# Performance work log

Hardware: AMD Instinct MI355X
Metric: run time of the kernel (lower is better)

The kernel has to match this reference:

```python
import jax, jax.numpy as jnp
import numpy as np

WS = (3, 8, 8)          # (t, h, w) window
SHIFT = (0, 4, 4)
HEADS = 6
DIM = 120
HD = DIM // HEADS
SCALE = HD ** -0.5
N = WS[0] * WS[1] * WS[2]   # 192 tokens per window
NQ = N // 3                 # 64 query tokens (last frame)


def _rel_pos_index():
    cd, ch, cw = np.arange(WS[0]), np.arange(WS[1]), np.arange(WS[2])
    c2 = np.stack(np.meshgrid(cd, ch, cw, indexing='ij')).reshape(3, -1)      # (3, N)
    c1 = np.stack(np.meshgrid(np.arange(1), ch, cw, indexing='ij')).reshape(3, -1)  # (3, NQ)
    rel = (c1[:, :, None] - c2[:, None, :]).transpose(1, 2, 0)                # (NQ, N, 3)
    rel = rel + np.array([WS[0] - 1, WS[1] - 1, WS[2] - 1])
    idx = rel[..., 0] * (2 * WS[1] - 1) * (2 * WS[2] - 1) + rel[..., 1] * (2 * WS[2] - 1) + rel[..., 2]
    return idx.astype(np.int32)  # values in [0, 3*15*15)


def _shift_attn_mask(h, w):
    # standard Swin shifted-window mask, tiled over the 3 frames
    img = np.zeros((h, w), np.int32)
    cnt = 0
    for hs in (slice(0, -WS[1]), slice(-WS[1], -SHIFT[1]), slice(-SHIFT[1], None)):
        for ws_ in (slice(0, -WS[2]), slice(-WS[2], -SHIFT[2]), slice(-SHIFT[2], None)):
            img[hs, ws_] = cnt
            cnt += 1
    win = img.reshape(h // WS[1], WS[1], w // WS[2], WS[2]).transpose(0, 2, 1, 3).reshape(-1, WS[1] * WS[2])
    m2 = win[:, None, :] - win[:, :, None]
    m2 = np.where(m2 != 0, -100.0, 0.0).astype(np.float32)  # (nW, 64, 64)
    return np.tile(m2, (1, 3, 3))                            # (nW, 192, 192)


def setup_inputs() -> dict:
    key = jax.random.key(0)
    ks = jax.random.split(key, 10)
    b, t, h, w, c = 1, 3, 256, 256, DIM
    nW = (h // WS[1]) * (w // WS[2])
    B_ = b * nW
    return {
        'x': jax.random.normal(ks[0], (b, t, h, w, c), jnp.float32),
        'quary0': jax.random.normal(ks[1], (B_, NQ, c), jnp.float32),
        'quary1': jax.random.normal(ks[2], (B_, NQ, c), jnp.float32),
        'qkv_w': jax.random.normal(ks[3], (3 * c, c), jnp.float32) * 0.02,
        'qkv_b': jnp.zeros((3 * c,), jnp.float32),
        'proj_w': jax.random.normal(ks[4], (c, c), jnp.float32) * 0.02,
        'proj_b': jnp.zeros((c,), jnp.float32),
        'rpb_table': jax.random.normal(ks[5], (WS[0] * (2 * WS[1] - 1) * (2 * WS[2] - 1), HEADS), jnp.float32) * 0.02,
        'pm_w': jax.random.normal(ks[6], (1, c), jnp.float32) * 0.02,
        'pm_b': jnp.zeros((1,), jnp.float32),
        'attn_mask': jnp.asarray(_shift_attn_mask(h, w)),
        'rel_idx': jnp.asarray(_rel_pos_index()),
    }


def reference(x, quary0, quary1, qkv_w, qkv_b, proj_w, proj_b, rpb_table, pm_w, pm_b, attn_mask, rel_idx):
    b, t, h, w, c = x.shape
    # cyclic shift
    x = jnp.roll(x, (-SHIFT[0], -SHIFT[1], -SHIFT[2]), axis=(1, 2, 3))
    # window partition -> (B_, N, c)
    xw = x.reshape(b, t // WS[0], WS[0], h // WS[1], WS[1], w // WS[2], WS[2], c)
    xw = xw.transpose(0, 1, 3, 5, 2, 4, 6, 7).reshape(-1, N, c)
    B_ = xw.shape[0]
    # adaptive mask prediction (eval path: hard threshold; sigmoid(s/T)>=0.5 <=> s>=0)
    pred_q = jax.lax.stop_gradient(xw[:, 2 * NQ:, :])
    soft = jnp.abs(pred_q - quary0) @ pm_w.T + pm_b          # (B_, NQ, 1)
    pred = (soft >= 0).astype(x.dtype)
    # qkv
    qkv = (xw @ qkv_w.T + qkv_b).reshape(B_, N, 3, HEADS, HD).transpose(2, 0, 3, 1, 4)
    q = qkv[0][:, :, 2 * NQ:, :] * SCALE                      # (B_, H, NQ, hd)
    k, v = qkv[1], qkv[2]                                     # (B_, H, N, hd)
    attn = jnp.einsum('bhqd,bhkd->bhqk', q, k)                # (B_, H, NQ, N)
    # gathered relative position bias
    rpb = rpb_table[rel_idx.reshape(-1)].reshape(NQ, N, HEADS).transpose(2, 0, 1)
    attn = attn + rpb[None]
    # shift mask
    nW = attn_mask.shape[0]
    attn = attn.reshape(b, nW, HEADS, NQ, N) + attn_mask[None, :, None, 2 * NQ:, :]
    attn = jax.nn.softmax(attn.reshape(B_, HEADS, NQ, N), axis=-1)
    out = jnp.einsum('bhqk,bhkd->bqhd', attn, v).reshape(B_, NQ, c)
    # output projection + token-pruning blend (math-equivalent to gather/fill eval path)
    x1 = out @ proj_w.T + proj_b
    x_pred = x1 * pred + quary1 * (1.0 - pred)
    xo = jnp.concatenate([x_pred, pred], axis=-1)             # (B_, NQ, c+1)
    # single-frame window reverse
    xo = xo.reshape(b, h // WS[1], w // WS[2], WS[1], WS[2], c + 1)
    xo = xo.transpose(0, 1, 3, 2, 4, 5).reshape(b, h, w, c + 1)
    xo = jnp.roll(xo, (SHIFT[1], SHIFT[2]), axis=(1, 2))
    return xo
```

## Files before the change

kernel.cpp:

```cpp
#include <hip/hip_runtime.h>
#include <math.h>

#define NT 256

typedef __attribute__((ext_vector_type(8))) short s16x8;
typedef __attribute__((ext_vector_type(4))) float f32x4;

#define KVF_OFF 0
#define QF_OFF  73728
#define PJF_OFF 122880
#define RPB_OFF 172032

__device__ __forceinline__ unsigned short f2bf(float f) {
    union { float f; unsigned int i; } v; v.f = f;
    unsigned int x = v.i;
    x += 0x7fffu + ((x >> 16) & 1u);
    return (unsigned short)(x >> 16);
}
__device__ __forceinline__ unsigned int pk2(float a, float b) {
    return (unsigned int)f2bf(a) | ((unsigned int)f2bf(b) << 16);
}

#define MFMA(a, b, c) __builtin_amdgcn_mfma_f32_16x16x32_bf16(a, b, c, 0, 0, 0)

__global__ void prep(const float* __restrict__ qkv_w,
                     const float* __restrict__ proj_w,
                     const float* __restrict__ rpb_table,
                     const int*   __restrict__ rel_idx,
                     unsigned char* __restrict__ wsb)
{
    int gid = blockIdx.x * blockDim.x + threadIdx.x;
    int nthr = gridDim.x * blockDim.x;
    unsigned short* KVF = (unsigned short*)(wsb + KVF_OFF);
    unsigned short* QF  = (unsigned short*)(wsb + QF_OFF);
    unsigned short* PJF = (unsigned short*)(wsb + PJF_OFF);
    float*          RPB = (float*)(wsb + RPB_OFF);

    for (int f = gid; f < 6 * 3 * 4 * 512; f += nthr) {
        int q = f & 511, rest = f >> 9;
        int kk = rest & 3, rest2 = rest >> 2;
        int nt = rest2 % 3, h = rest2 / 3;
        int ln = q >> 3, j = q & 7;
        int l15 = ln & 15, qd = ln >> 4;
        int nglob = nt * 16 + l15, k = kk * 32 + qd * 8 + j;
        float v = 0.f;
        if (k < 120 && nglob < 40) {
            int row = (nglob < 20) ? (120 + h * 20 + nglob) : (240 + h * 20 + nglob - 20);
            v = qkv_w[row * 120 + k];
        }
        KVF[f] = f2bf(v);
    }
    for (int f = gid; f < 6 * 2 * 4 * 512; f += nthr) {
        int q = f & 511, rest = f >> 9;
        int kk = rest & 3, rest2 = rest >> 2;
        int nt = rest2 & 1, h = rest2 >> 1;
        int ln = q >> 3, j = q & 7;
        int l15 = ln & 15, qd = ln >> 4;
        int nn = nt * 16 + l15, k = kk * 32 + qd * 8 + j;
        int row = h * 20 + nn;
        float v = (k < 120) ? qkv_w[row * 120 + k] : 0.f;
        QF[f] = f2bf(v);
    }
    for (int f = gid; f < 6 * 8 * 512; f += nthr) {
        int q = f & 511, rest = f >> 9;
        int ct = rest & 7, h = rest >> 3;
        int ln = q >> 3, j = q & 7;
        int l15 = ln & 15, qd = ln >> 4;
        int c = ct * 16 + l15, k = qd * 8 + j;
        float v = (k < 20 && c < 120) ? proj_w[c * 120 + h * 20 + k] : 0.f;
        PJF[f] = f2bf(v);
    }
    for (int i = gid; i < 6 * 192 * 64; i += nthr) {
        int r = i & 63, n = (i >> 6) % 192, h = i / (192 * 64);
        RPB[i] = rpb_table[rel_idx[r * 192 + n] * 6 + h];
    }
}

__global__ __launch_bounds__(NT, 2)
void swin_mfma(const float* __restrict__ x,
               const float* __restrict__ quary0,
               const float* __restrict__ quary1,
               const float* __restrict__ qkv_b,
               const float* __restrict__ proj_b,
               const float* __restrict__ pm_w,
               const float* __restrict__ pm_b,
               const unsigned char* __restrict__ wsb,
               float* __restrict__ out)
{
    __shared__ alignas(16) unsigned char smem[79888];
    unsigned short* xw = (unsigned short*)smem;
    unsigned short* ks = (unsigned short*)(smem + 46096);
    unsigned short* vt = (unsigned short*)(smem + 61456);
    unsigned short* qs = (unsigned short*)(smem + 74256);
    float* pred_s = (float*)(smem + 79376);
    int*   grp_s  = (int*)(smem + 79632);

    const int tid = threadIdx.x;
    const int wv = tid >> 6, ln = tid & 63;
    const int l15 = ln & 15, qd = ln >> 4;
    const int widx = blockIdx.x;
    const int wh = widx >> 5, ww = widx & 31;
    const float SCALE = 0.22360679774997896f;

    const unsigned short* KVF = (const unsigned short*)(wsb + KVF_OFF);
    const unsigned short* QF  = (const unsigned short*)(wsb + QF_OFF);
    const unsigned short* PJF = (const unsigned short*)(wsb + PJF_OFF);
    const float*          RPB = (const float*)(wsb + RPB_OFF);

    for (int e = tid; e < 192 * 30; e += NT) {
        int n = e / 30, c4 = e % 30;
        int f = n >> 6, ii = (n >> 3) & 7, jj = n & 7;
        int y0 = (wh * 8 + ii + 4) & 255;
        int x0 = (ww * 8 + jj + 4) & 255;
        float4 val = *(const float4*)(x + (((size_t)(f * 256 + y0)) * 256 + x0) * 120 + c4 * 4);
        unsigned int lo = (unsigned)f2bf(val.x) | ((unsigned)f2bf(val.y) << 16);
        unsigned int hi = (unsigned)f2bf(val.z) | ((unsigned)f2bf(val.w) << 16);
        unsigned int off = (unsigned)(n * 120 + c4 * 4);
        *(unsigned int*)(xw + off)     = lo;
        *(unsigned int*)(xw + off + 2) = hi;
    }
    if (tid < 8) xw[192 * 120 + tid] = 0;
    for (int e = tid; e < 192 * 12; e += NT) ks[(e / 12) * 40 + 20 + (e % 12)] = 0;
    for (int e = tid; e < 64 * 12;  e += NT) qs[(e / 12) * 40 + 20 + (e % 12)] = 0;
    for (int e = tid; e < 12 * 200; e += NT) vt[(20 + e / 200) * 200 + (e % 200)] = 0;
    if (tid < 64) {
        int ii = tid >> 3, jj = tid & 7;
        int y0 = (wh * 8 + ii + 4) & 255;
        int x0 = (ww * 8 + jj + 4) & 255;
        int hg = (y0 >= 248) + (y0 >= 252);
        int wg = (x0 >= 248) + (x0 >= 252);
        grp_s[tid] = hg * 3 + wg;
    }
    {
        int r = tid >> 2, j = tid & 3;
        int ii = r >> 3, jj = r & 7;
        int y0 = (wh * 8 + ii + 4) & 255;
        int x0 = (ww * 8 + jj + 4) & 255;
        const float* xr  = x + (((size_t)(2 * 256 + y0)) * 256 + x0) * 120;
        const float* q0r = quary0 + ((size_t)widx * 64 + r) * 120;
        float acc = 0.f;
        for (int ch = j * 30; ch < j * 30 + 30; ++ch)
            acc += fabsf(xr[ch] - q0r[ch]) * pm_w[ch];
        acc += __shfl_xor(acc, 1);
        acc += __shfl_xor(acc, 2);
        if (j == 0) pred_s[r] = (acc + pm_b[0] >= 0.f) ? 1.f : 0.f;
    }
    __syncthreads();

    const int q_l = wv * 16 + l15;
    const int gq = grp_s[q_l];
    unsigned long long mbits = 0ull;
    #pragma unroll
    for (int t = 0; t < 12; ++t)
        #pragma unroll
        for (int r = 0; r < 4; ++r) {
            int tok = t * 16 + qd * 4 + r;
            if (gq != grp_s[tok & 63]) mbits |= (1ull << (t * 4 + r));
        }
    const int srcA = (((qd * 2) & 3) << 4) | l15;
    const int srcB = (((qd * 2 + 1) & 3) << 4) | l15;
    const int msel = qd >> 1;

    f32x4 pacc[8];
    #pragma unroll
    for (int i = 0; i < 8; ++i) { f32x4 z = {0.f,0.f,0.f,0.f}; pacc[i] = z; }

    for (int h = 0; h < 6; ++h) {
        for (int e = wv; e < 44; e += 4) {
            if (e < 36) {
                int mt = e % 12, nt = e / 12;
                const unsigned short* arow  = xw + (mt * 16 + l15) * 120;
                const unsigned short* bbase = KVF + ((h * 3 + nt) * 4) * 512 + ln * 8;
                f32x4 acc = {0.f, 0.f, 0.f, 0.f};
                #pragma unroll
                for (int kk = 0; kk < 4; ++kk) {
                    s16x8 aF = *(const s16x8*)(arow + kk * 32 + qd * 8);
                    s16x8 bF = *(const s16x8*)(bbase + kk * 512);
                    acc = MFMA(aF, bF, acc);
                }
                int nglob = nt * 16 + l15;
                if (nglob < 40) {
                    float bias = qkv_b[nglob < 20 ? (120 + h * 20 + nglob)
                                                  : (240 + h * 20 + nglob - 20)];
                    #pragma unroll
                    for (int reg = 0; reg < 4; ++reg) {
                        int tok = mt * 16 + qd * 4 + reg;
                        unsigned short vb = f2bf(acc[reg] + bias);
                        if (nglob < 20) ks[tok * 40 + nglob] = vb;
                        else            vt[(nglob - 20) * 200 + tok] = vb;
                    }
                }
            } else {
                int t = e - 36, mt = t & 3, nt = t >> 2;
                const unsigned short* arow  = xw + (128 + mt * 16 + l15) * 120;
                const unsigned short* bbase = QF + ((h * 2 + nt) * 4) * 512 + ln * 8;
                f32x4 acc = {0.f, 0.f, 0.f, 0.f};
                #pragma unroll
                for (int kk = 0; kk < 4; ++kk) {
                    s16x8 aF = *(const s16x8*)(arow + kk * 32 + qd * 8);
                    s16x8 bF = *(const s16x8*)(bbase + kk * 512);
                    acc = MFMA(aF, bF, acc);
                }
                int nn = nt * 16 + l15;
                if (nn < 20) {
                    float bias = qkv_b[h * 20 + nn];
                    #pragma unroll
                    for (int reg = 0; reg < 4; ++reg)
                        qs[(mt * 16 + qd * 4 + reg) * 40 + nn] = f2bf((acc[reg] + bias) * SCALE);
                }
            }
        }
        __syncthreads();

        const float* rbase = RPB + ((size_t)(h * 192 + qd * 4)) * 64 + q_l;
        float vals[48];
        #pragma unroll
        for (int t = 0; t < 12; ++t)
            #pragma unroll
            for (int r = 0; r < 4; ++r)
                vals[t * 4 + r] = rbase[(t * 16 + r) * 64]
                                + (((mbits >> (t * 4 + r)) & 1ull) ? -100.f : 0.f);

        const s16x8 bQ = *(const s16x8*)(qs + q_l * 40 + qd * 8);
        f32x4 sc[12];
        #pragma unroll
        for (int t = 0; t < 12; ++t) {
            s16x8 aK = *(const s16x8*)(ks + (t * 16 + l15) * 40 + qd * 8);
            f32x4 z = {0.f, 0.f, 0.f, 0.f};
            sc[t] = MFMA(aK, bQ, z);
        }

        float m = -1e30f;
        #pragma unroll
        for (int t = 0; t < 12; ++t)
            #pragma unroll
            for (int r = 0; r < 4; ++r) {
                float v = vals[t * 4 + r] + sc[t][r];
                vals[t * 4 + r] = v; m = fmaxf(m, v);
            }
        m = fmaxf(m, __shfl_xor(m, 16));
        m = fmaxf(m, __shfl_xor(m, 32));
        float s = 0.f;
        #pragma unroll
        for (int i = 0; i < 48; ++i) { float ev = __expf(vals[i] - m); vals[i] = ev; s += ev; }
        s += __shfl_xor(s, 16);
        s += __shfl_xor(s, 32);
        float inv = 1.0f / s;

        unsigned int plo[12], phi[12];
        #pragma unroll
        for (int t = 0; t < 12; ++t) {
            plo[t] = pk2(vals[t * 4 + 0] * inv, vals[t * 4 + 1] * inv);
            phi[t] = pk2(vals[t * 4 + 2] * inv, vals[t * 4 + 3] * inv);
        }

        f32x4 o0 = {0.f,0.f,0.f,0.f}, o1 = {0.f,0.f,0.f,0.f};
        #pragma unroll
        for (int kk = 0; kk < 6; ++kk) {
            unsigned int a0 = __shfl(plo[2 * kk],     srcA);
            unsigned int a1 = __shfl(plo[2 * kk + 1], srcA);
            unsigned int b0 = __shfl(phi[2 * kk],     srcA);
            unsigned int b1 = __shfl(phi[2 * kk + 1], srcA);
            unsigned int c0 = __shfl(plo[2 * kk],     srcB);
            unsigned int c1 = __shfl(plo[2 * kk + 1], srcB);
            unsigned int d0 = __shfl(phi[2 * kk],     srcB);
            unsigned int d1 = __shfl(phi[2 * kk + 1], srcB);
            union { s16x8 v; unsigned int u[4]; } bf;
            bf.u[0] = msel ? a1 : a0;
            bf.u[1] = msel ? b1 : b0;
            bf.u[2] = msel ? c1 : c0;
            bf.u[3] = msel ? d1 : d0;
            s16x8 aV0 = *(const s16x8*)(vt + l15 * 200 + kk * 32 + qd * 8);
            s16x8 aV1 = *(const s16x8*)(vt + (16 + l15) * 200 + kk * 32 + qd * 8);
            o0 = MFMA(aV0, bf.v, o0);
            o1 = MFMA(aV1, bf.v, o1);
        }

        {
            unsigned int ol0 = pk2(o0[0], o0[1]), oh0 = pk2(o0[2], o0[3]);
            unsigned int ol1 = pk2(o1[0], o1[1]), oh1 = pk2(o1[2], o1[3]);
            unsigned int w0a = __shfl(ol0, srcA), w0b = __shfl(ol1, srcA);
            unsigned int w1a = __shfl(oh0, srcA), w1b = __shfl(oh1, srcA);
            unsigned int w2a = __shfl(ol0, srcB), w2b = __shfl(ol1, srcB);
            unsigned int w3a = __shfl(oh0, srcB), w3b = __shfl(oh1, srcB);
            union { s16x8 v; unsigned int u[4]; } bo;
            bo.u[0] = msel ? w0b : w0a;
            bo.u[1] = msel ? w1b : w1a;
            bo.u[2] = msel ? w2b : w2a;
            bo.u[3] = msel ? w3b : w3a;
            #pragma unroll
            for (int ct = 0; ct < 8; ++ct) {
                s16x8 aP = *(const s16x8*)(PJF + (h * 8 + ct) * 512 + ln * 8);
                pacc[ct] = MFMA(aP, bo.v, pacc[ct]);
            }
        }
        __syncthreads();
    }

    float* xo = (float*)smem;
    #pragma unroll
    for (int ct = 0; ct < 8; ++ct)
        #pragma unroll
        for (int r = 0; r < 4; ++r) {
            int c = ct * 16 + qd * 4 + r;
            if (c < 120) xo[q_l * 129 + c] = pacc[ct][r];
        }
    __syncthreads();

    for (int e = tid; e < 64 * 121; e += NT) {
        int r = e / 121, c = e - r * 121;
        int ii = r >> 3, jj = r & 7;
        int y0 = (wh * 8 + ii + 4) & 255;
        int x0 = (ww * 8 + jj + 4) & 255;
        float p = pred_s[r];
        float val;
        if (c < 120)
            val = (p != 0.f) ? (xo[r * 129 + c] + proj_b[c])
                             : quary1[(size_t)widx * 7680 + (size_t)r * 120 + c];
        else
            val = p;
        out[((size_t)(y0 * 256 + x0)) * 121 + c] = val;
    }
}

extern "C" void kernel_launch(void* const* d_in, const int* in_sizes, int n_in,
                              void* d_out, int out_size, void* d_ws, size_t ws_size,
                              hipStream_t stream) {
    const float* x        = (const float*)d_in[0];
    const float* quary0   = (const float*)d_in[1];
    const float* quary1   = (const float*)d_in[2];
    const float* qkv_w    = (const float*)d_in[3];
    const float* qkv_b    = (const float*)d_in[4];
    const float* proj_w   = (const float*)d_in[5];
    const float* proj_b   = (const float*)d_in[6];
    const float* rpb      = (const float*)d_in[7];
    const float* pm_w     = (const float*)d_in[8];
    const float* pm_b     = (const float*)d_in[9];
    const int*   rel_idx  = (const int*)d_in[11];
    float* out = (float*)d_out;
    unsigned char* wsb = (unsigned char*)d_ws;

    prep<<<128, 512, 0, stream>>>(qkv_w, proj_w, rpb, rel_idx, wsb);
    swin_mfma<<<1024, NT, 0, stream>>>(x, quary0, quary1, qkv_b, proj_b,
                                       pm_w, pm_b, wsb, out);
}
```

Measured before the change: 457.8 us.

## Hoist QKV projection for all heads before attention and split heads across waves

Q, K and V are now projected for all six heads in one upfront MFMA pass into large LDS buffers, replacing the per-head projection loop that needed two block syncs per head. The softmax scale is folded into the Q weights and bias. The block doubles to 512 threads, with two wave groups each taking three heads. Their projection partial sums are written to two LDS tiles and added in the epilogue. LDS grows to about 159KB, and launch_bounds(512,2) may squeeze registers, so there is a risk of spills or lost occupancy.

```diff
diff --git a/kernel.cpp b/kernel.cpp
--- a/kernel.cpp
+++ b/kernel.cpp
@@ -1,15 +1,17 @@
 #include <hip/hip_runtime.h>
 #include <math.h>
 
-#define NT 256
+#define NT 512
 
 typedef __attribute__((ext_vector_type(8))) short s16x8;
+typedef __attribute__((ext_vector_type(4))) short s16x4;
 typedef __attribute__((ext_vector_type(4))) float f32x4;
 
-#define KVF_OFF 0
-#define QF_OFF  73728
-#define PJF_OFF 122880
-#define RPB_OFF 172032
+#define WKT_OFF 0
+#define WVT_OFF 32768
+#define WQT_OFF 65536
+#define PJF_OFF 102400
+#define RPB_OFF 151552
 
 __device__ __forceinline__ unsigned short f2bf(float f) {
     union { float f; unsigned int i; } v; v.f = f;
@@ -31,41 +33,42 @@
 {
     int gid = blockIdx.x * blockDim.x + threadIdx.x;
     int nthr = gridDim.x * blockDim.x;
-    unsigned short* KVF = (unsigned short*)(wsb + KVF_OFF);
-    unsigned short* QF  = (unsigned short*)(wsb + QF_OFF);
+    unsigned short* WKT = (unsigned short*)(wsb + WKT_OFF);
+    unsigned short* WVT = (unsigned short*)(wsb + WVT_OFF);
+    unsigned short* WQT = (unsigned short*)(wsb + WQT_OFF);
     unsigned short* PJF = (unsigned short*)(wsb + PJF_OFF);
     float*          RPB = (float*)(wsb + RPB_OFF);
 
-    for (int f = gid; f < 6 * 3 * 4 * 512; f += nthr) {
+    for (int f = gid; f < 8 * 4 * 512; f += nthr) {
         int q = f & 511, rest = f >> 9;
-        int kk = rest & 3, rest2 = rest >> 2;
-        int nt = rest2 % 3, h = rest2 / 3;
-        int ln = q >> 3, j = q & 7;
-        int l15 = ln & 15, qd = ln >> 4;
-        int nglob = nt * 16 + l15, k = kk * 32 + qd * 8 + j;
-        float v = 0.f;
-        if (k < 120 && nglob < 40) {
-            int row = (nglob < 20) ? (120 + h * 20 + nglob) : (240 + h * 20 + nglob - 20);
-            v = qkv_w[row * 120 + k];
-        }
-        KVF[f] = f2bf(v);
-    }
-    for (int f = gid; f < 6 * 2 * 4 * 512; f += nthr) {
+        int kk = rest & 3, nt = rest >> 2;
+        int ln = q >> 3, j = q & 7, l15 = ln & 15, qd = ln >> 4;
+        int c = nt * 16 + l15, ch = kk * 32 + qd * 8 + j;
+        float v = (c < 120 && ch < 120) ? qkv_w[(120 + c) * 120 + ch] : 0.f;
+        WKT[f] = f2bf(v);
+    }
+    for (int f = gid; f < 8 * 4 * 512; f += nthr) {
         int q = f & 511, rest = f >> 9;
-        int kk = rest & 3, rest2 = rest >> 2;
-        int nt = rest2 & 1, h = rest2 >> 1;
-        int ln = q >> 3, j = q & 7;
-        int l15 = ln & 15, qd = ln >> 4;
-        int nn = nt * 16 + l15, k = kk * 32 + qd * 8 + j;
-        int row = h * 20 + nn;
-        float v = (k < 120) ? qkv_w[row * 120 + k] : 0.f;
-        QF[f] = f2bf(v);
+        int kk = rest & 3, mt = rest >> 2;
+        int ln = q >> 3, j = q & 7, l15 = ln & 15, qd = ln >> 4;
+        int d = mt * 16 + l15, ch = kk * 32 + qd * 8 + j;
+        float v = (d < 120 && ch < 120) ? qkv_w[(240 + d) * 120 + ch] : 0.f;
+        WVT[f] = f2bf(v);
+    }
+    for (int f = gid; f < 9 * 4 * 512; f += nthr) {
+        int q = f & 511, rest = f >> 9;
+        int kk = rest & 3, nt = rest >> 2;
+        int ln = q >> 3, j = q & 7, l15 = ln & 15, qd = ln >> 4;
+        int c = nt * 16 + l15, ch = kk * 32 + qd * 8 + j;
+        int hh = (c * 171) >> 12, rel = c - hh * 24;
+        float v = (rel < 20 && ch < 120)
+                    ? qkv_w[(hh * 20 + rel) * 120 + ch] * 0.22360679774997896f : 0.f;
+        WQT[f] = f2bf(v);
     }
     for (int f = gid; f < 6 * 8 * 512; f += nthr) {
         int q = f & 511, rest = f >> 9;
         int ct = rest & 7, h = rest >> 3;
-        int ln = q >> 3, j = q & 7;
-        int l15 = ln & 15, qd = ln >> 4;
+        int ln = q >> 3, j = q & 7, l15 = ln & 15, qd = ln >> 4;
         int c = ct * 16 + l15, k = qd * 8 + j;
         float v = (k < 20 && c < 120) ? proj_w[c * 120 + h * 20 + k] : 0.f;
         PJF[f] = f2bf(v);
@@ -87,23 +90,23 @@
                const unsigned char* __restrict__ wsb,
                float* __restrict__ out)
 {
-    __shared__ alignas(16) unsigned char smem[79888];
+    __shared__ alignas(16) unsigned char smem[159152];
     unsigned short* xw = (unsigned short*)smem;
-    unsigned short* ks = (unsigned short*)(smem + 46096);
-    unsigned short* vt = (unsigned short*)(smem + 61456);
-    unsigned short* qs = (unsigned short*)(smem + 74256);
-    float* pred_s = (float*)(smem + 79376);
-    int*   grp_s  = (int*)(smem + 79632);
+    unsigned short* kd = (unsigned short*)(smem + 46096);
+    unsigned short* vt = (unsigned short*)(smem + 92208);
+    unsigned short* qp = (unsigned short*)(smem + 140208);
+    float* pred_s = (float*)(smem + 158640);
+    int*   grp_s  = (int*)(smem + 158896);
 
     const int tid = threadIdx.x;
     const int wv = tid >> 6, ln = tid & 63;
     const int l15 = ln & 15, qd = ln >> 4;
     const int widx = blockIdx.x;
     const int wh = widx >> 5, ww = widx & 31;
-    const float SCALE = 0.22360679774997896f;
-
-    const unsigned short* KVF = (const unsigned short*)(wsb + KVF_OFF);
-    const unsigned short* QF  = (const unsigned short*)(wsb + QF_OFF);
+
+    const unsigned short* WKT = (const unsigned short*)(wsb + WKT_OFF);
+    const unsigned short* WVT = (const unsigned short*)(wsb + WVT_OFF);
+    const unsigned short* WQT = (const unsigned short*)(wsb + WQT_OFF);
     const unsigned short* PJF = (const unsigned short*)(wsb + PJF_OFF);
     const float*          RPB = (const float*)(wsb + RPB_OFF);
 
@@ -119,10 +122,8 @@
         *(unsigned int*)(xw + off)     = lo;
         *(unsigned int*)(xw + off + 2) = hi;
     }
-    if (tid < 8) xw[192 * 120 + tid] = 0;
-    for (int e = tid; e < 192 * 12; e += NT) ks[(e / 12) * 40 + 20 + (e % 12)] = 0;
-    for (int e = tid; e < 64 * 12;  e += NT) qs[(e / 12) * 40 + 20 + (e % 12)] = 0;
-    for (int e = tid; e < 12 * 200; e += NT) vt[(20 + e / 200) * 200 + (e % 200)] = 0;
+    if (tid < 8)  xw[192 * 120 + tid] = 0;
+    if (tid < 16) kd[192 * 120 + tid] = 0;
     if (tid < 64) {
         int ii = tid >> 3, jj = tid & 7;
         int y0 = (wh * 8 + ii + 4) & 255;
@@ -131,7 +132,7 @@
         int wg = (x0 >= 248) + (x0 >= 252);
         grp_s[tid] = hg * 3 + wg;
     }
-    {
+    if (tid < 256) {
         int r = tid >> 2, j = tid & 3;
         int ii = r >> 3, jj = r & 7;
         int y0 = (wh * 8 + ii + 4) & 255;
@@ -147,7 +148,71 @@
     }
     __syncthreads();
 
-    const int q_l = wv * 16 + l15;
+    for (int e = wv; e < 48; e += 8) {
+        int mt = e >> 2, ntp = e & 3;
+        const unsigned short* arow = xw + (mt * 16 + l15) * 120;
+        const unsigned short* b0 = WKT + (2 * ntp) * 4 * 512 + ln * 8;
+        f32x4 a0 = {0.f,0.f,0.f,0.f}, a1 = {0.f,0.f,0.f,0.f};
+        #pragma unroll
+        for (int kk = 0; kk < 4; ++kk) {
+            s16x8 aF = *(const s16x8*)(arow + kk * 32 + qd * 8);
+            a0 = MFMA(aF, *(const s16x8*)(b0 + kk * 512), a0);
+            a1 = MFMA(aF, *(const s16x8*)(b0 + 2048 + kk * 512), a1);
+        }
+        #pragma unroll
+        for (int half = 0; half < 2; ++half) {
+            int c = (2 * ntp + half) * 16 + l15;
+            f32x4 acc = half ? a1 : a0;
+            if (c < 120) {
+                float bias = qkv_b[120 + c];
+                #pragma unroll
+                for (int reg = 0; reg < 4; ++reg)
+                    kd[(mt * 16 + qd * 4 + reg) * 120 + c] = f2bf(acc[reg] + bias);
+            }
+        }
+    }
+    for (int e = wv; e < 48; e += 8) {
+        int nt = e >> 2, mtp = e & 3;
+        const unsigned short* brow = xw + (nt * 16 + l15) * 120;
+        const unsigned short* a0 = WVT + (2 * mtp) * 4 * 512 + ln * 8;
+        f32x4 c0 = {0.f,0.f,0.f,0.f}, c1 = {0.f,0.f,0.f,0.f};
+        #pragma unroll
+        for (int kk = 0; kk < 4; ++kk) {
+            s16x8 bF = *(const s16x8*)(brow + kk * 32 + qd * 8);
+            c0 = MFMA(*(const s16x8*)(a0 + kk * 512), bF, c0);
+            c1 = MFMA(*(const s16x8*)(a0 + 2048 + kk * 512), bF, c1);
+        }
+        #pragma unroll
+        for (int half = 0; half < 2; ++half) {
+            f32x4 acc = half ? c1 : c0;
+            #pragma unroll
+            for (int reg = 0; reg < 4; ++reg) {
+                int d = (2 * mtp + half) * 16 + qd * 4 + reg;
+                if (d < 120)
+                    vt[d * 200 + nt * 16 + l15] = f2bf(acc[reg] + qkv_b[240 + d]);
+            }
+        }
+    }
+    for (int e = wv; e < 36; e += 8) {
+        int mt = e / 9, nt = e - mt * 9;
+        const unsigned short* arow = xw + (128 + mt * 16 + l15) * 120;
+        const unsigned short* b0 = WQT + nt * 4 * 512 + ln * 8;
+        f32x4 acc = {0.f,0.f,0.f,0.f};
+        #pragma unroll
+        for (int kk = 0; kk < 4; ++kk)
+            acc = MFMA(*(const s16x8*)(arow + kk * 32 + qd * 8),
+                       *(const s16x8*)(b0 + kk * 512), acc);
+        int c = nt * 16 + l15;
+        int hh = (c * 171) >> 12, rel = c - hh * 24;
+        float bias = (rel < 20) ? qkv_b[hh * 20 + rel] * 0.22360679774997896f : 0.f;
+        #pragma unroll
+        for (int reg = 0; reg < 4; ++reg)
+            qp[(mt * 16 + qd * 4 + reg) * 144 + c] = f2bf(acc[reg] + bias);
+    }
+    __syncthreads();
+
+    const int qt = wv & 3, hp = wv >> 2;
+    const int q_l = qt * 16 + l15;
     const int gq = grp_s[q_l];
     unsigned long long mbits = 0ull;
     #pragma unroll
@@ -165,52 +230,8 @@
     #pragma unroll
     for (int i = 0; i < 8; ++i) { f32x4 z = {0.f,0.f,0.f,0.f}; pacc[i] = z; }
 
-    for (int h = 0; h < 6; ++h) {
-        for (int e = wv; e < 44; e += 4) {
-            if (e < 36) {
-                int mt = e % 12, nt = e / 12;
-                const unsigned short* arow  = xw + (mt * 16 + l15) * 120;
-                const unsigned short* bbase = KVF + ((h * 3 + nt) * 4) * 512 + ln * 8;
-                f32x4 acc = {0.f, 0.f, 0.f, 0.f};
-                #pragma unroll
-                for (int kk = 0; kk < 4; ++kk) {
-                    s16x8 aF = *(const s16x8*)(arow + kk * 32 + qd * 8);
-                    s16x8 bF = *(const s16x8*)(bbase + kk * 512);
-                    acc = MFMA(aF, bF, acc);
-                }
-                int nglob = nt * 16 + l15;
-                if (nglob < 40) {
-                    float bias = qkv_b[nglob < 20 ? (120 + h * 20 + nglob)
-                                                  : (240 + h * 20 + nglob - 20)];
-                    #pragma unroll
-                    for (int reg = 0; reg < 4; ++reg) {
-                        int tok = mt * 16 + qd * 4 + reg;
-                        unsigned short vb = f2bf(acc[reg] + bias);
-                        if (nglob < 20) ks[tok * 40 + nglob] = vb;
-                        else            vt[(nglob - 20) * 200 + tok] = vb;
-                    }
-                }
-            } else {
-                int t = e - 36, mt = t & 3, nt = t >> 2;
-                const unsigned short* arow  = xw + (128 + mt * 16 + l15) * 120;
-                const unsigned short* bbase = QF + ((h * 2 + nt) * 4) * 512 + ln * 8;
-                f32x4 acc = {0.f, 0.f, 0.f, 0.f};
-                #pragma unroll
-                for (int kk = 0; kk < 4; ++kk) {
-                    s16x8 aF = *(const s16x8*)(arow + kk * 32 + qd * 8);
-                    s16x8 bF = *(const s16x8*)(bbase + kk * 512);
-                    acc = MFMA(aF, bF, acc);
-                }
-                int nn = nt * 16 + l15;
-                if (nn < 20) {
-                    float bias = qkv_b[h * 20 + nn];
-                    #pragma unroll
-                    for (int reg = 0; reg < 4; ++reg)
-                        qs[(mt * 16 + qd * 4 + reg) * 40 + nn] = f2bf((acc[reg] + bias) * SCALE);
-                }
-            }
-        }
-        __syncthreads();
+    for (int jj = 0; jj < 3; ++jj) {
+        const int h = hp + 2 * jj;
 
         const float* rbase = RPB + ((size_t)(h * 192 + qd * 4)) * 64 + q_l;
         float vals[48];
@@ -221,13 +242,20 @@
                 vals[t * 4 + r] = rbase[(t * 16 + r) * 64]
                                 + (((mbits >> (t * 4 + r)) & 1ull) ? -100.f : 0.f);
 
-        const s16x8 bQ = *(const s16x8*)(qs + q_l * 40 + qd * 8);
+        s16x8 zf = {0,0,0,0,0,0,0,0};
+        int koff = (qd == 3) ? 0 : qd * 8;
+        s16x8 bQl = *(const s16x8*)(qp + q_l * 144 + h * 24 + koff);
+        s16x8 bQ = (qd == 3) ? zf : bQl;
+
         f32x4 sc[12];
         #pragma unroll
         for (int t = 0; t < 12; ++t) {
-            s16x8 aK = *(const s16x8*)(ks + (t * 16 + l15) * 40 + qd * 8);
-            f32x4 z = {0.f, 0.f, 0.f, 0.f};
-            sc[t] = MFMA(aK, bQ, z);
+            const unsigned short* kp = kd + (t * 16 + l15) * 120 + h * 20 + qd * 8;
+            union { s16x8 v8; s16x4 v4[2]; } ak;
+            ak.v4[0] = *(const s16x4*)(kp);
+            ak.v4[1] = *(const s16x4*)(kp + 4);
+            f32x4 z = {0.f,0.f,0.f,0.f};
+            sc[t] = MFMA(ak.v8, bQ, z);
         }
 
         float m = -1e30f;
@@ -270,8 +298,8 @@
             bf.u[1] = msel ? b1 : b0;
             bf.u[2] = msel ? c1 : c0;
             bf.u[3] = msel ? d1 : d0;
-            s16x8 aV0 = *(const s16x8*)(vt + l15 * 200 + kk * 32 + qd * 8);
-            s16x8 aV1 = *(const s16x8*)(vt + (16 + l15) * 200 + kk * 32 + qd * 8);
+            s16x8 aV0 = *(const s16x8*)(vt + (h * 20 + l15) * 200 + kk * 32 + qd * 8);
+            s16x8 aV1 = *(const s16x8*)(vt + (h * 20 + 16 + l15) * 200 + kk * 32 + qd * 8);
             o0 = MFMA(aV0, bf.v, o0);
             o1 = MFMA(aV1, bf.v, o1);
         }
@@ -294,19 +322,23 @@
                 pacc[ct] = MFMA(aP, bo.v, pacc[ct]);
             }
         }
-        __syncthreads();
-    }
-
-    float* xo = (float*)smem;
-    #pragma unroll
-    for (int ct = 0; ct < 8; ++ct)
-        #pragma unroll
-        for (int r = 0; r < 4; ++r) {
-            int c = ct * 16 + qd * 4 + r;
-            if (c < 120) xo[q_l * 129 + c] = pacc[ct][r];
-        }
+    }
     __syncthreads();
 
+    {
+        float* xo = (float*)(smem + ((wv < 4) ? 0u : 46096u));
+        #pragma unroll
+        for (int ct = 0; ct < 8; ++ct)
+            #pragma unroll
+            for (int reg = 0; reg < 4; ++reg) {
+                int c = ct * 16 + qd * 4 + reg;
+                if (c < 120) xo[q_l * 129 + c] = pacc[ct][reg];
+            }
+    }
+    __syncthreads();
+
+    const float* x1p = (const float*)smem;
+    const float* x2p = (const float*)(smem + 46096);
     for (int e = tid; e < 64 * 121; e += NT) {
         int r = e / 121, c = e - r * 121;
         int ii = r >> 3, jj = r & 7;
@@ -315,7 +347,7 @@
         float p = pred_s[r];
         float val;
         if (c < 120)
-            val = (p != 0.f) ? (xo[r * 129 + c] + proj_b[c])
+            val = (p != 0.f) ? (x1p[r * 129 + c] + x2p[r * 129 + c] + proj_b[c])
                              : quary1[(size_t)widx * 7680 + (size_t)r * 120 + c];
         else
             val = p;
@@ -331,8 +363,8 @@
     const float* quary1   = (const float*)d_in[2];
     const float* qkv_w    = (const float*)d_in[3];
     const float* qkv_b    = (const float*)d_in[4];
+    const float* proj_b   = (const float*)d_in[6];
     const float* proj_w   = (const float*)d_in[5];
-    const float* proj_b   = (const float*)d_in[6];
     const float* rpb      = (const float*)d_in[7];
     const float* pm_w     = (const float*)d_in[8];
     const float* pm_b     = (const float*)d_in[9];
```

Measured after the change: 561.6 us. 1.23x slower.

## Drop shared-memory x staging and read x from global inside QKV MFMA loop

Applied to the files above, without the earlier changes.

Removes the bf16 copy of the window's x tile from LDS and instead loads fp32 x directly from global memory inside the QKV projection, converting to bf16 per MFMA operand. This shrinks LDS from about 78KB to 33KB and raises launch bounds to four blocks per SM for higher occupancy. The trade-off is that x is reloaded and reconverted from global for every head and every N-tile (6 heads × 3 tiles for K/V, 6 heads × 2 tiles for Q), so global/L2 traffic and conversion ALU work rise substantially.

```diff
diff --git a/kernel.cpp b/kernel.cpp
--- a/kernel.cpp
+++ b/kernel.cpp
@@ -19,6 +19,14 @@
 }
 __device__ __forceinline__ unsigned int pk2(float a, float b) {
     return (unsigned int)f2bf(a) | ((unsigned int)f2bf(b) << 16);
+}
+__device__ __forceinline__ s16x8 cvt8(float4 a, float4 b) {
+    union { unsigned int u[4]; s16x8 v; } r;
+    r.u[0] = pk2(a.x, a.y);
+    r.u[1] = pk2(a.z, a.w);
+    r.u[2] = pk2(b.x, b.y);
+    r.u[3] = pk2(b.z, b.w);
+    return r.v;
 }
 
 #define MFMA(a, b, c) __builtin_amdgcn_mfma_f32_16x16x32_bf16(a, b, c, 0, 0, 0)
@@ -76,7 +84,7 @@
     }
 }
 
-__global__ __launch_bounds__(NT, 2)
+__global__ __launch_bounds__(NT, 4)
 void swin_mfma(const float* __restrict__ x,
                const float* __restrict__ quary0,
                const float* __restrict__ quary1,
@@ -87,13 +95,12 @@
                const unsigned char* __restrict__ wsb,
                float* __restrict__ out)
 {
-    __shared__ alignas(16) unsigned char smem[79888];
-    unsigned short* xw = (unsigned short*)smem;
-    unsigned short* ks = (unsigned short*)(smem + 46096);
-    unsigned short* vt = (unsigned short*)(smem + 61456);
-    unsigned short* qs = (unsigned short*)(smem + 74256);
-    float* pred_s = (float*)(smem + 79376);
-    int*   grp_s  = (int*)(smem + 79632);
+    __shared__ alignas(16) unsigned char smem[33792];
+    unsigned short* ks = (unsigned short*)smem;
+    unsigned short* vt = (unsigned short*)(smem + 15360);
+    unsigned short* qs = (unsigned short*)(smem + 28160);
+    float* pred_s = (float*)(smem + 33280);
+    int*   grp_s  = (int*)(smem + 33536);
 
     const int tid = threadIdx.x;
     const int wv = tid >> 6, ln = tid & 63;
@@ -107,19 +114,6 @@
     const unsigned short* PJF = (const unsigned short*)(wsb + PJF_OFF);
     const float*          RPB = (const float*)(wsb + RPB_OFF);
 
-    for (int e = tid; e < 192 * 30; e += NT) {
-        int n = e / 30, c4 = e % 30;
-        int f = n >> 6, ii = (n >> 3) & 7, jj = n & 7;
-        int y0 = (wh * 8 + ii + 4) & 255;
-        int x0 = (ww * 8 + jj + 4) & 255;
-        float4 val = *(const float4*)(x + (((size_t)(f * 256 + y0)) * 256 + x0) * 120 + c4 * 4);
-        unsigned int lo = (unsigned)f2bf(val.x) | ((unsigned)f2bf(val.y) << 16);
-        unsigned int hi = (unsigned)f2bf(val.z) | ((unsigned)f2bf(val.w) << 16);
-        unsigned int off = (unsigned)(n * 120 + c4 * 4);
-        *(unsigned int*)(xw + off)     = lo;
-        *(unsigned int*)(xw + off + 2) = hi;
-    }
-    if (tid < 8) xw[192 * 120 + tid] = 0;
     for (int e = tid; e < 192 * 12; e += NT) ks[(e / 12) * 40 + 20 + (e % 12)] = 0;
     for (int e = tid; e < 64 * 12;  e += NT) qs[(e / 12) * 40 + 20 + (e % 12)] = 0;
     for (int e = tid; e < 12 * 200; e += NT) vt[(20 + e / 200) * 200 + (e % 200)] = 0;
@@ -169,14 +163,21 @@
         for (int e = wv; e < 44; e += 4) {
             if (e < 36) {
                 int mt = e % 12, nt = e / 12;
-                const unsigned short* arow  = xw + (mt * 16 + l15) * 120;
+                int n = mt * 16 + l15;
+                int f = n >> 6, ii = (n >> 3) & 7, jj = n & 7;
+                int y0 = (wh * 8 + ii + 4) & 255;
+                int x0 = (ww * 8 + jj + 4) & 255;
+                const float* xr = x + (((size_t)(f * 256 + y0)) * 256 + x0) * 120;
                 const unsigned short* bbase = KVF + ((h * 3 + nt) * 4) * 512 + ln * 8;
                 f32x4 acc = {0.f, 0.f, 0.f, 0.f};
                 #pragma unroll
                 for (int kk = 0; kk < 4; ++kk) {
-                    s16x8 aF = *(const s16x8*)(arow + kk * 32 + qd * 8);
-                    s16x8 bF = *(const s16x8*)(bbase + kk * 512);
-                    acc = MFMA(aF, bF, acc);
+                    float4 va = {0.f,0.f,0.f,0.f}, vb = {0.f,0.f,0.f,0.f};
+                    if (!(kk == 3 && qd == 3)) {
+                        va = *(const float4*)(xr + kk * 32 + qd * 8);
+                        vb = *(const float4*)(xr + kk * 32 + qd * 8 + 4);
+                    }
+                    acc = MFMA(cvt8(va, vb), *(const s16x8*)(bbase + kk * 512), acc);
                 }
                 int nglob = nt * 16 + l15;
                 if (nglob < 40) {
@@ -185,21 +186,28 @@
                     #pragma unroll
                     for (int reg = 0; reg < 4; ++reg) {
                         int tok = mt * 16 + qd * 4 + reg;
-                        unsigned short vb = f2bf(acc[reg] + bias);
-                        if (nglob < 20) ks[tok * 40 + nglob] = vb;
-                        else            vt[(nglob - 20) * 200 + tok] = vb;
+                        unsigned short vbf = f2bf(acc[reg] + bias);
+                        if (nglob < 20) ks[tok * 40 + nglob] = vbf;
+                        else            vt[(nglob - 20) * 200 + tok] = vbf;
                     }
                 }
             } else {
                 int t = e - 36, mt = t & 3, nt = t >> 2;
-                const unsigned short* arow  = xw + (128 + mt * 16 + l15) * 120;
+                int n = 128 + mt * 16 + l15;
+                int f = n >> 6, ii = (n >> 3) & 7, jj = n & 7;
+                int y0 = (wh * 8 + ii + 4) & 255;
+                int x0 = (ww * 8 + jj + 4) & 255;
+                const float* xr = x + (((size_t)(f * 256 + y0)) * 256 + x0) * 120;
                 const unsigned short* bbase = QF + ((h * 2 + nt) * 4) * 512 + ln * 8;
                 f32x4 acc = {0.f, 0.f, 0.f, 0.f};
                 #pragma unroll
                 for (int kk = 0; kk < 4; ++kk) {
-                    s16x8 aF = *(const s16x8*)(arow + kk * 32 + qd * 8);
-                    s16x8 bF = *(const s16x8*)(bbase + kk * 512);
-                    acc = MFMA(aF, bF, acc);
+                    float4 va = {0.f,0.f,0.f,0.f}, vb = {0.f,0.f,0.f,0.f};
+                    if (!(kk == 3 && qd == 3)) {
+                        va = *(const float4*)(xr + kk * 32 + qd * 8);
+                        vb = *(const float4*)(xr + kk * 32 + qd * 8 + 4);
+                    }
+                    acc = MFMA(cvt8(va, vb), *(const s16x8*)(bbase + kk * 512), acc);
                 }
                 int nn = nt * 16 + l15;
                 if (nn < 20) {
```

Result: slower. 673.0 us (+47.0%).

## Software-pipeline per-head QKV projection with double-buffered V/Q in LDS

Applied to the files above, without the earlier changes.

Moves the QKV projection for head h+1 into the attention loop of head h. Q and V get double buffers, and the K tile is overwritten only after a barrier that follows the score MFMAs. This removes one barrier per head and overlaps the projection MFMAs with softmax and PV work. K and Q row strides shrink from 40 to 24 and the zero-padding is trimmed, which lowers LDS use. The risk is heavier register pressure and subtle ordering hazards on the shared K buffer.

```diff
diff --git a/kernel.cpp b/kernel.cpp
--- a/kernel.cpp
+++ b/kernel.cpp
@@ -87,13 +87,13 @@
                const unsigned char* __restrict__ wsb,
                float* __restrict__ out)
 {
-    __shared__ alignas(16) unsigned char smem[79888];
+    __shared__ alignas(16) unsigned char smem[77968];
     unsigned short* xw = (unsigned short*)smem;
     unsigned short* ks = (unsigned short*)(smem + 46096);
+    unsigned short* qs = (unsigned short*)(smem + 55312);
     unsigned short* vt = (unsigned short*)(smem + 61456);
-    unsigned short* qs = (unsigned short*)(smem + 74256);
-    float* pred_s = (float*)(smem + 79376);
-    int*   grp_s  = (int*)(smem + 79632);
+    float* pred_s = (float*)(smem + 77456);
+    int*   grp_s  = (int*)(smem + 77712);
 
     const int tid = threadIdx.x;
     const int wv = tid >> 6, ln = tid & 63;
@@ -113,16 +113,16 @@
         int y0 = (wh * 8 + ii + 4) & 255;
         int x0 = (ww * 8 + jj + 4) & 255;
         float4 val = *(const float4*)(x + (((size_t)(f * 256 + y0)) * 256 + x0) * 120 + c4 * 4);
-        unsigned int lo = (unsigned)f2bf(val.x) | ((unsigned)f2bf(val.y) << 16);
-        unsigned int hi = (unsigned)f2bf(val.z) | ((unsigned)f2bf(val.w) << 16);
+        unsigned int lo = pk2(val.x, val.y);
+        unsigned int hi = pk2(val.z, val.w);
         unsigned int off = (unsigned)(n * 120 + c4 * 4);
         *(unsigned int*)(xw + off)     = lo;
         *(unsigned int*)(xw + off + 2) = hi;
     }
     if (tid < 8) xw[192 * 120 + tid] = 0;
-    for (int e = tid; e < 192 * 12; e += NT) ks[(e / 12) * 40 + 20 + (e % 12)] = 0;
-    for (int e = tid; e < 64 * 12;  e += NT) qs[(e / 12) * 40 + 20 + (e % 12)] = 0;
-    for (int e = tid; e < 12 * 200; e += NT) vt[(20 + e / 200) * 200 + (e % 200)] = 0;
+    for (int e = tid; e < 192 * 4; e += NT) ks[(e >> 2) * 24 + 20 + (e & 3)] = 0;
+    for (int e = tid; e < 2 * 64 * 4; e += NT)
+        qs[(e >> 8) * 1536 + ((e >> 2) & 63) * 24 + 20 + (e & 3)] = 0;
     if (tid < 64) {
         int ii = tid >> 3, jj = tid & 7;
         int y0 = (wh * 8 + ii + 4) & 255;
@@ -147,6 +147,51 @@
     }
     __syncthreads();
 
+    auto kvjob = [&](int mt, int nt, int hh, int pty) {
+        const unsigned short* arow  = xw + (mt * 16 + l15) * 120;
+        const unsigned short* bbase = KVF + ((hh * 3 + nt) * 4) * 512 + ln * 8;
+        f32x4 acc = {0.f, 0.f, 0.f, 0.f};
+        #pragma unroll
+        for (int kk = 0; kk < 4; ++kk)
+            acc = MFMA(*(const s16x8*)(arow + kk * 32 + qd * 8),
+                       *(const s16x8*)(bbase + kk * 512), acc);
+        int nglob = nt * 16 + l15;
+        if (nglob < 40) {
+            float bias = qkv_b[nglob < 20 ? (120 + hh * 20 + nglob)
+                                          : (240 + hh * 20 + nglob - 20)];
+            #pragma unroll
+            for (int reg = 0; reg < 4; ++reg) {
+                int tok = mt * 16 + qd * 4 + reg;
+                unsigned short vb = f2bf(acc[reg] + bias);
+                if (nglob < 20) ks[tok * 24 + nglob] = vb;
+                else            vt[pty * 4000 + (nglob - 20) * 200 + tok] = vb;
+            }
+        }
+    };
+    auto qjob = [&](int mt, int nt, int hh, int pty) {
+        const unsigned short* arow  = xw + (128 + mt * 16 + l15) * 120;
+        const unsigned short* bbase = QF + ((hh * 2 + nt) * 4) * 512 + ln * 8;
+        f32x4 acc = {0.f, 0.f, 0.f, 0.f};
+        #pragma unroll
+        for (int kk = 0; kk < 4; ++kk)
+            acc = MFMA(*(const s16x8*)(arow + kk * 32 + qd * 8),
+                       *(const s16x8*)(bbase + kk * 512), acc);
+        int nn = nt * 16 + l15;
+        if (nn < 20) {
+            float bias = qkv_b[hh * 20 + nn];
+            #pragma unroll
+            for (int reg = 0; reg < 4; ++reg)
+                qs[pty * 1536 + (mt * 16 + qd * 4 + reg) * 24 + nn] =
+                    f2bf((acc[reg] + bias) * SCALE);
+        }
+    };
+
+    for (int e = wv; e < 44; e += 4) {
+        if (e < 36) kvjob(e % 12, e / 12, 0, 0);
+        else        { int t = e - 36; qjob(t & 3, t >> 2, 0, 0); }
+    }
+    __syncthreads();
+
     const int q_l = wv * 16 + l15;
     const int gq = grp_s[q_l];
     unsigned long long mbits = 0ull;
@@ -160,57 +205,14 @@
     const int srcA = (((qd * 2) & 3) << 4) | l15;
     const int srcB = (((qd * 2 + 1) & 3) << 4) | l15;
     const int msel = qd >> 1;
+    const s16x8 zf = {0, 0, 0, 0, 0, 0, 0, 0};
 
     f32x4 pacc[8];
     #pragma unroll
     for (int i = 0; i < 8; ++i) { f32x4 z = {0.f,0.f,0.f,0.f}; pacc[i] = z; }
 
     for (int h = 0; h < 6; ++h) {
-        for (int e = wv; e < 44; e += 4) {
-            if (e < 36) {
-                int mt = e % 12, nt = e / 12;
-                const unsigned short* arow  = xw + (mt * 16 + l15) * 120;
-                const unsigned short* bbase = KVF + ((h * 3 + nt) * 4) * 512 + ln * 8;
-                f32x4 acc = {0.f, 0.f, 0.f, 0.f};
-                #pragma unroll
-                for (int kk = 0; kk < 4; ++kk) {
-                    s16x8 aF = *(const s16x8*)(arow + kk * 32 + qd * 8);
-                    s16x8 bF = *(const s16x8*)(bbase + kk * 512);
-                    acc = MFMA(aF, bF, acc);
-                }
-                int nglob = nt * 16 + l15;
-                if (nglob < 40) {
-                    float bias = qkv_b[nglob < 20 ? (120 + h * 20 + nglob)
-                                                  : (240 + h * 20 + nglob - 20)];
-                    #pragma unroll
-                    for (int reg = 0; reg < 4; ++reg) {
-                        int tok = mt * 16 + qd * 4 + reg;
-                        unsigned short vb = f2bf(acc[reg] + bias);
-                        if (nglob < 20) ks[tok * 40 + nglob] = vb;
-                        else            vt[(nglob - 20) * 200 + tok] = vb;
-                    }
-                }
-            } else {
-                int t = e - 36, mt = t & 3, nt = t >> 2;
-                const unsigned short* arow  = xw + (128 + mt * 16 + l15) * 120;
-                const unsigned short* bbase = QF + ((h * 2 + nt) * 4) * 512 + ln * 8;
-                f32x4 acc = {0.f, 0.f, 0.f, 0.f};
-                #pragma unroll
-                for (int kk = 0; kk < 4; ++kk) {
-                    s16x8 aF = *(const s16x8*)(arow + kk * 32 + qd * 8);
-                    s16x8 bF = *(const s16x8*)(bbase + kk * 512);
-                    acc = MFMA(aF, bF, acc);
-                }
-                int nn = nt * 16 + l15;
-                if (nn < 20) {
-                    float bias = qkv_b[h * 20 + nn];
-                    #pragma unroll
-                    for (int reg = 0; reg < 4; ++reg)
-                        qs[(mt * 16 + qd * 4 + reg) * 40 + nn] = f2bf((acc[reg] + bias) * SCALE);
-                }
-            }
-        }
-        __syncthreads();
+        const int pr = h & 1, pw = (h + 1) & 1;
 
         const float* rbase = RPB + ((size_t)(h * 192 + qd * 4)) * 64 + q_l;
         float vals[48];
@@ -221,15 +223,22 @@
                 vals[t * 4 + r] = rbase[(t * 16 + r) * 64]
                                 + (((mbits >> (t * 4 + r)) & 1ull) ? -100.f : 0.f);
 
-        const s16x8 bQ = *(const s16x8*)(qs + q_l * 40 + qd * 8);
+        if (h < 5) {
+            for (int e = wv; e < 20; e += 4) {
+                if (e < 12) kvjob(e, 2, h + 1, pw);
+                else        { int t = e - 12; qjob(t & 3, t >> 2, h + 1, pw); }
+            }
+        }
+
+        s16x8 bQ = zf;
+        if (qd < 3) bQ = *(const s16x8*)(qs + pr * 1536 + q_l * 24 + qd * 8);
         f32x4 sc[12];
         #pragma unroll
         for (int t = 0; t < 12; ++t) {
-            s16x8 aK = *(const s16x8*)(ks + (t * 16 + l15) * 40 + qd * 8);
+            s16x8 aK = *(const s16x8*)(ks + (t * 16 + l15) * 24 + qd * 8);
             f32x4 z = {0.f, 0.f, 0.f, 0.f};
             sc[t] = MFMA(aK, bQ, z);
         }
-
         float m = -1e30f;
         #pragma unroll
         for (int t = 0; t < 12; ++t)
@@ -240,6 +249,13 @@
             }
         m = fmaxf(m, __shfl_xor(m, 16));
         m = fmaxf(m, __shfl_xor(m, 32));
+        __syncthreads();
+
+        if (h < 5) {
+            for (int e = wv; e < 24; e += 4)
+                kvjob(e % 12, (e < 12) ? 0 : 1, h + 1, pw);
+        }
+
         float s = 0.f;
         #pragma unroll
         for (int i = 0; i < 48; ++i) { float ev = __expf(vals[i] - m); vals[i] = ev; s += ev; }
@@ -270,8 +286,10 @@
             bf.u[1] = msel ? b1 : b0;
             bf.u[2] = msel ? c1 : c0;
             bf.u[3] = msel ? d1 : d0;
-            s16x8 aV0 = *(const s16x8*)(vt + l15 * 200 + kk * 32 + qd * 8);
-            s16x8 aV1 = *(const s16x8*)(vt + (16 + l15) * 200 + kk * 32 + qd * 8);
+            s16x8 aV0 = *(const s16x8*)(vt + pr * 4000 + l15 * 200 + kk * 32 + qd * 8);
+            s16x8 aV1 = zf;
+            if (l15 < 4)
+                aV1 = *(const s16x8*)(vt + pr * 4000 + (16 + l15) * 200 + kk * 32 + qd * 8);
             o0 = MFMA(aV0, bf.v, o0);
             o1 = MFMA(aV1, bf.v, o1);
         }
```

Result: faster. 436.0 us (-4.8%).
